# Performance work log

Hardware: AMD Instinct MI355X
Metric: run time of the kernel (lower is better)

Reference implementation:

```python
import jax, jax.numpy as jnp
import numpy as np
from jax import lax

T, B, D, H = 512, 64, 256, 512  # time, batch, input_dim, hidden_dim


def setup_inputs() -> dict:
    key = jax.random.key(0)
    ks = jax.random.split(key, 9)
    fan_in = D + H
    s = 1.0 / np.sqrt(fan_in)
    inputs = jax.random.normal(ks[0], (T, B, D), dtype=jnp.float32)
    # torch nn.Linear weight layout: [out_features, in_features]
    Wf = jax.random.uniform(ks[1], (H, fan_in), jnp.float32, -s, s)
    bf = jax.random.uniform(ks[2], (H,), jnp.float32, -s, s)
    Wi = jax.random.uniform(ks[3], (H, fan_in), jnp.float32, -s, s)
    bi = jax.random.uniform(ks[4], (H,), jnp.float32, -s, s)
    Wg = jax.random.uniform(ks[5], (H, fan_in), jnp.float32, -s, s)
    bg = jax.random.uniform(ks[6], (H,), jnp.float32, -s, s)
    Wo = jax.random.uniform(ks[7], (H, fan_in), jnp.float32, -s, s)
    bo = jax.random.uniform(ks[8], (H,), jnp.float32, -s, s)
    return {"inputs": inputs, "Wf": Wf, "bf": bf, "Wi": Wi, "bi": bi,
            "Wg": Wg, "bg": bg, "Wo": Wo, "bo": bo}


def reference(inputs, Wf, bf, Wi, bi, Wg, bg, Wo, bo):
    # LSTM-style gated recurrence, n_qubits=0 path (no depth loop, proj_back = Identity)
    batch = inputs.shape[1]
    hidden = bf.shape[0]
    h0 = jnp.zeros((batch, hidden), inputs.dtype)
    c0 = jnp.zeros((batch, hidden), inputs.dtype)

    def step(carry, x):
        hx, cx = carry
        comb = jnp.concatenate([x, hx], axis=1)  # [B, D+H]
        f = jax.nn.sigmoid(comb @ Wf.T + bf)
        i = jax.nn.sigmoid(comb @ Wi.T + bi)
        g = jnp.tanh(comb @ Wg.T + bg)
        o = jax.nn.sigmoid(comb @ Wo.T + bo)
        cx = f * cx + i * g
        hx = o * jnp.tanh(cx)
        return (hx, cx), hx

    (hx, cx), outputs = lax.scan(step, (h0, c0), inputs)
    return outputs, hx, cx
```

## Files before the change

### kernel.cpp

```cpp
#include <hip/hip_runtime.h>
#include <stdint.h>

#define T_STEPS 512
#define BATCH   64
#define DIN     256
#define HID     512
#define KTOT    768
#define NTEAMS  4
#define TB      16
#define KK_X    8
#define KK_H    16
#define KK_ALL  24

typedef __bf16 v8bf __attribute__((ext_vector_type(8)));
typedef float  v4f  __attribute__((ext_vector_type(4)));
typedef unsigned int v4u __attribute__((ext_vector_type(4)));

#define FLAGS_OFF 0
#define HBUF_OFF  8192
#define WPK_OFF   (HBUF_OFF + 131072)
#define XPK_OFF   (WPK_OFF + 3145728)

#define LOADH(d, a, IMM) \
  asm volatile("global_load_dwordx4 %0, %1, off offset:" IMM " sc0 sc1" \
               : "=v"(d) : "v"(a) : "memory")
#define STORE_SHORT_C(a, v) \
  asm volatile("global_store_short %0, %1, off sc0 sc1" :: "v"(a), "v"(v) : "memory")
#define STORE_DWORD_C(a, v) \
  asm volatile("global_store_dword %0, %1, off sc0 sc1" :: "v"(a), "v"(v) : "memory")
#define DRAIN_VM() asm volatile("s_waitcnt vmcnt(0)" ::: "memory")

static __device__ __forceinline__ unsigned short f2bf(float x) {
  union { float f; uint32_t u; } v; v.f = x;
  uint32_t r = (v.u + 0x7fffu + ((v.u >> 16) & 1u)) >> 16;
  return (unsigned short)r;
}

static __device__ __forceinline__ float sigm(float x) {
  float e = __builtin_amdgcn_exp2f(-1.44269504f * x);
  return __builtin_amdgcn_rcpf(1.0f + e);
}
static __device__ __forceinline__ float tanh_(float x) {
  float e = __builtin_amdgcn_exp2f(2.88539008f * x);
  return 1.0f - 2.0f * __builtin_amdgcn_rcpf(e + 1.0f);
}

__global__ void pack_w(const float* __restrict__ Wf, const float* __restrict__ Wi,
                       const float* __restrict__ Wg, const float* __restrict__ Wo,
                       unsigned short* __restrict__ wpk) {
  int n = blockIdx.x * 256 + threadIdx.x;
  int l  = n & 63;
  int kk = (n >> 6) % KK_ALL;
  int wv = (n >> 6) / KK_ALL;
  int row  = l & 15;
  int gate = row & 3;
  int unit = (wv >> 2) * 16 + (wv & 3) * 4 + (row >> 2);
  int col  = kk * 32 + (l >> 4) * 8;
  const float* W = (gate == 0) ? Wf : (gate == 1) ? Wi : (gate == 2) ? Wg : Wo;
  const float* src = W + (size_t)unit * KTOT + col;
  unsigned short* dst = wpk + (size_t)n * 8;
#pragma unroll
  for (int e = 0; e < 8; e++) dst[e] = f2bf(src[e]);
}

__global__ void pack_x(const float* __restrict__ X, unsigned short* __restrict__ xpk) {
  int n = blockIdx.x * 256 + threadIdx.x;
  int l    = n & 63;
  int kk   = (n >> 6) & 7;
  int team = (n >> 9) & 3;
  int t    = n >> 11;
  int b    = team * TB + (l & 15);
  int col  = kk * 32 + (l >> 4) * 8;
  const float* src = X + ((size_t)(t * BATCH + b)) * DIN + col;
  unsigned short* dst = xpk + (size_t)n * 8;
#pragma unroll
  for (int e = 0; e < 8; e++) dst[e] = f2bf(src[e]);
}

__global__ void __launch_bounds__(256, 1)
lstm_rec(const float* __restrict__ bf_, const float* __restrict__ bi_,
         const float* __restrict__ bg_, const float* __restrict__ bo_,
         const unsigned short* __restrict__ wpk, const unsigned short* __restrict__ xpk,
         float* __restrict__ out, unsigned int* flags, unsigned short* hbuf) {
  int blk  = blockIdx.x;
  int team = blk & 7;
  if (team >= NTEAMS) return;
  int cu  = blk >> 3;
  int tid = threadIdx.x;
  int w   = tid >> 6, l = tid & 63;
  int brow = l & 15;
  int ul   = l >> 4;
  int u    = cu * 16 + w * 4 + ul;
  int bglob = team * TB + brow;

  v4u wfu[KK_ALL];
  {
    const v4u* wp = (const v4u*)(wpk + ((size_t)(cu * 4 + w)) * (KK_ALL * 512) + l * 8);
#pragma unroll
    for (int kk = 0; kk < KK_ALL; kk++) wfu[kk] = wp[kk * 64];
#pragma unroll
    for (int kk = 0; kk < KK_ALL; kk++) asm volatile("" : "+v"(wfu[kk]));
  }
  float b0 = bf_[u], b1 = bi_[u], b2 = bg_[u], b3 = bo_[u];
  float c = 0.0f, hval = 0.0f;

  char* slab0 = (char*)(hbuf + (size_t)team * 2 * (TB * HID));
  char* slab1 = slab0 + TB * HID * 2;
  const char* cons0 = slab0 + brow * 1024 + ul * 16;
  const char* cons1 = slab1 + brow * 1024 + ul * 16;
  char* pub0 = slab0 + brow * 1024 + u * 2;
  char* pub1 = slab1 + brow * 1024 + u * 2;

  unsigned int* ftm = flags + (size_t)team * 32 * 16;
  unsigned int* myflag = ftm + (size_t)cu * 16;
  const unsigned int* pollp = ftm + (size_t)(l & 31) * 16;

  float* outb = out + (size_t)bglob * HID + u;

  for (int t = 0; t < T_STEPS; t++) {
    v8bf xf[KK_X];
    {
      const v8bf* xp = (const v8bf*)(xpk + ((size_t)(t * NTEAMS + team)) * (KK_X * 512) + l * 8);
#pragma unroll
      for (int kk = 0; kk < KK_X; kk++) xf[kk] = xp[kk * 64];
    }

    if (t > 0) {
      if (w == 0) {
        while (true) {
          unsigned int v = __hip_atomic_load(pollp, __ATOMIC_RELAXED, __HIP_MEMORY_SCOPE_AGENT);
          if (__all(v >= (unsigned)t)) break;
        }
      }
      __syncthreads();
    }

    const char* cb = (t & 1) ? cons1 : cons0;
    v4u hf[16];
    LOADH(hf[0],  cb, "0");   LOADH(hf[1],  cb, "64");
    LOADH(hf[2],  cb, "128"); LOADH(hf[3],  cb, "192");
    LOADH(hf[4],  cb, "256"); LOADH(hf[5],  cb, "320");
    LOADH(hf[6],  cb, "384"); LOADH(hf[7],  cb, "448");
    LOADH(hf[8],  cb, "512"); LOADH(hf[9],  cb, "576");
    LOADH(hf[10], cb, "640"); LOADH(hf[11], cb, "704");
    LOADH(hf[12], cb, "768"); LOADH(hf[13], cb, "832");
    LOADH(hf[14], cb, "896"); LOADH(hf[15], cb, "960");

    v4f acc[4];
    acc[0] = (v4f){b0, b1, b2, b3};
    acc[1] = (v4f){0.f, 0.f, 0.f, 0.f};
    acc[2] = (v4f){0.f, 0.f, 0.f, 0.f};
    acc[3] = (v4f){0.f, 0.f, 0.f, 0.f};
#pragma unroll
    for (int kk = 0; kk < KK_X; kk++)
      acc[kk & 3] = __builtin_amdgcn_mfma_f32_16x16x32_bf16(
          __builtin_bit_cast(v8bf, wfu[kk]), xf[kk], acc[kk & 3], 0, 0, 0);

    DRAIN_VM();
    __builtin_amdgcn_sched_barrier(0);

#pragma unroll
    for (int kk = 0; kk < KK_H; kk++)
      acc[kk & 3] = __builtin_amdgcn_mfma_f32_16x16x32_bf16(
          __builtin_bit_cast(v8bf, wfu[KK_X + kk]),
          __builtin_bit_cast(v8bf, hf[kk]), acc[kk & 3], 0, 0, 0);

    v4f g4 = (acc[0] + acc[1]) + (acc[2] + acc[3]);

    float fg = sigm(g4[0]);
    float ig = sigm(g4[1]);
    float gg = tanh_(g4[2]);
    float og = sigm(g4[3]);
    c    = fg * c + ig * gg;
    hval = og * tanh_(c);

    outb[(size_t)t * (BATCH * HID)] = hval;

    {
      char* pd = ((t + 1) & 1) ? pub1 : pub0;
      unsigned int hb = f2bf(hval);
      STORE_SHORT_C(pd, hb);
    }
    DRAIN_VM();
    __syncthreads();
    if (tid == 0) {
      unsigned int fv = (unsigned)(t + 1);
      STORE_DWORD_C(myflag, fv);
    }
  }

  float* hx = out + (size_t)T_STEPS * BATCH * HID;
  hx[(size_t)bglob * HID + u] = hval;
  float* cx = hx + BATCH * HID;
  cx[(size_t)bglob * HID + u] = c;
}

extern "C" void kernel_launch(void* const* d_in, const int* in_sizes, int n_in,
                              void* d_out, int out_size, void* d_ws, size_t ws_size,
                              hipStream_t stream) {
  const float* X  = (const float*)d_in[0];
  const float* Wf = (const float*)d_in[1];
  const float* bf = (const float*)d_in[2];
  const float* Wi = (const float*)d_in[3];
  const float* bi = (const float*)d_in[4];
  const float* Wg = (const float*)d_in[5];
  const float* bg = (const float*)d_in[6];
  const float* Wo = (const float*)d_in[7];
  const float* bo = (const float*)d_in[8];
  float* out = (float*)d_out;
  char* ws = (char*)d_ws;

  unsigned int*   flags = (unsigned int*)(ws + FLAGS_OFF);
  unsigned short* hbuf  = (unsigned short*)(ws + HBUF_OFF);
  unsigned short* wpk   = (unsigned short*)(ws + WPK_OFF);
  unsigned short* xpk   = (unsigned short*)(ws + XPK_OFF);

  hipMemsetAsync(ws, 0, WPK_OFF, stream);
  pack_w<<<768, 256, 0, stream>>>(Wf, Wi, Wg, Wo, wpk);
  pack_x<<<4096, 256, 0, stream>>>(X, xpk);
  lstm_rec<<<256, 256, 0, stream>>>(bf, bi, bg, bo, wpk, xpk, out, flags, hbuf);
}
```

Baseline: 1.652 ms.

## Stage recurrent h through LDS with coalesced loads and packed publishes

Each wave now loads one quarter of the team's h slab with four coalesced device-scope loads and writes it into swizzled shared memory. All waves then read their MFMA B fragments from LDS, so each wave no longer issues sixteen scattered global loads. On the publish side, values are gathered with shuffles so 16 lanes each write one packed 8-byte store instead of every lane storing a short. Cache-scope bits drop from sc0 sc1 to sc1, the publish and flag write are skipped on the last step, and a bounded poll loop is added; the extra __syncthreads and the weaker coherence scope are the main risks.

```diff
diff --git a/kernel.cpp b/kernel.cpp
--- a/kernel.cpp
+++ b/kernel.cpp
@@ -12,23 +12,35 @@
 #define KK_H    16
 #define KK_ALL  24
 
+#define POLL_BOUND (1 << 18)
+
 typedef __bf16 v8bf __attribute__((ext_vector_type(8)));
 typedef float  v4f  __attribute__((ext_vector_type(4)));
 typedef unsigned int v4u __attribute__((ext_vector_type(4)));
+typedef unsigned int v2u __attribute__((ext_vector_type(2)));
 
 #define FLAGS_OFF 0
 #define HBUF_OFF  8192
 #define WPK_OFF   (HBUF_OFF + 131072)
 #define XPK_OFF   (WPK_OFF + 3145728)
 
-#define LOADH(d, a, IMM) \
-  asm volatile("global_load_dwordx4 %0, %1, off offset:" IMM " sc0 sc1" \
+#define LOADX4_DEV(d, a, IMM) \
+  asm volatile("global_load_dwordx4 %0, %1, off offset:" IMM " sc1" \
                : "=v"(d) : "v"(a) : "memory")
-#define STORE_SHORT_C(a, v) \
-  asm volatile("global_store_short %0, %1, off sc0 sc1" :: "v"(a), "v"(v) : "memory")
-#define STORE_DWORD_C(a, v) \
-  asm volatile("global_store_dword %0, %1, off sc0 sc1" :: "v"(a), "v"(v) : "memory")
+#define ST2_DEV(a, v) \
+  asm volatile("global_store_dwordx2 %0, %1, off sc1" :: "v"(a), "v"(v) : "memory")
+#define ST_DW_DEV(a, v) \
+  asm volatile("global_store_dword %0, %1, off sc1" :: "v"(a), "v"(v) : "memory")
+#define LOADX4(d, a) \
+  asm volatile("global_load_dwordx4 %0, %1, off" : "=v"(d) : "v"(a) : "memory")
 #define DRAIN_VM() asm volatile("s_waitcnt vmcnt(0)" ::: "memory")
+
+static __device__ __forceinline__ unsigned int ld_flag_dev(const unsigned int* p) {
+  unsigned int v;
+  asm volatile("global_load_dword %0, %1, off sc1\n\ts_waitcnt vmcnt(0)"
+               : "=v"(v) : "v"(p) : "memory");
+  return v;
+}
 
 static __device__ __forceinline__ unsigned short f2bf(float x) {
   union { float f; uint32_t u; } v; v.f = x;
@@ -93,27 +105,24 @@
   int u    = cu * 16 + w * 4 + ul;
   int bglob = team * TB + brow;
 
+  __shared__ v4u hls[1024];
+  char* hl = (char*)hls;
+
   v4u wfu[KK_ALL];
   {
-    const v4u* wp = (const v4u*)(wpk + ((size_t)(cu * 4 + w)) * (KK_ALL * 512) + l * 8);
-#pragma unroll
-    for (int kk = 0; kk < KK_ALL; kk++) wfu[kk] = wp[kk * 64];
-#pragma unroll
-    for (int kk = 0; kk < KK_ALL; kk++) asm volatile("" : "+v"(wfu[kk]));
+    const char* wp = (const char*)(wpk + ((size_t)(cu * 4 + w)) * (KK_ALL * 512) + l * 8);
+#pragma unroll
+    for (int kk = 0; kk < KK_ALL; kk++) LOADX4(wfu[kk], wp + (size_t)kk * 1024);
+    DRAIN_VM();
   }
   float b0 = bf_[u], b1 = bi_[u], b2 = bg_[u], b3 = bo_[u];
   float c = 0.0f, hval = 0.0f;
 
   char* slab0 = (char*)(hbuf + (size_t)team * 2 * (TB * HID));
   char* slab1 = slab0 + TB * HID * 2;
-  const char* cons0 = slab0 + brow * 1024 + ul * 16;
-  const char* cons1 = slab1 + brow * 1024 + ul * 16;
-  char* pub0 = slab0 + brow * 1024 + u * 2;
-  char* pub1 = slab1 + brow * 1024 + u * 2;
 
   unsigned int* ftm = flags + (size_t)team * 32 * 16;
   unsigned int* myflag = ftm + (size_t)cu * 16;
-  const unsigned int* pollp = ftm + (size_t)(l & 31) * 16;
 
   float* outb = out + (size_t)bglob * HID + u;
 
@@ -127,24 +136,25 @@
 
     if (t > 0) {
       if (w == 0) {
+        const unsigned int* pp = ftm + (size_t)(l & 31) * 16;
+        int guard = 0;
         while (true) {
-          unsigned int v = __hip_atomic_load(pollp, __ATOMIC_RELAXED, __HIP_MEMORY_SCOPE_AGENT);
+          unsigned int v = ld_flag_dev(pp);
           if (__all(v >= (unsigned)t)) break;
+          if (++guard > POLL_BOUND) break;
         }
       }
       __syncthreads();
     }
 
-    const char* cb = (t & 1) ? cons1 : cons0;
-    v4u hf[16];
-    LOADH(hf[0],  cb, "0");   LOADH(hf[1],  cb, "64");
-    LOADH(hf[2],  cb, "128"); LOADH(hf[3],  cb, "192");
-    LOADH(hf[4],  cb, "256"); LOADH(hf[5],  cb, "320");
-    LOADH(hf[6],  cb, "384"); LOADH(hf[7],  cb, "448");
-    LOADH(hf[8],  cb, "512"); LOADH(hf[9],  cb, "576");
-    LOADH(hf[10], cb, "640"); LOADH(hf[11], cb, "704");
-    LOADH(hf[12], cb, "768"); LOADH(hf[13], cb, "832");
-    LOADH(hf[14], cb, "896"); LOADH(hf[15], cb, "960");
+    v4u s0, s1, s2, s3;
+    {
+      const char* sb = ((t & 1) ? slab1 : slab0) + w * 4096 + l * 16;
+      LOADX4_DEV(s0, sb, "0");
+      LOADX4_DEV(s1, sb, "1024");
+      LOADX4_DEV(s2, sb, "2048");
+      LOADX4_DEV(s3, sb, "3072");
+    }
 
     v4f acc[4];
     acc[0] = (v4f){b0, b1, b2, b3};
@@ -159,12 +169,22 @@
     DRAIN_VM();
     __builtin_amdgcn_sched_barrier(0);
 
-#pragma unroll
-    for (int kk = 0; kk < KK_H; kk++)
+    {
+      int r = w * 4;
+      *(v4u*)(hl + (((r + 0) * 1024 + l * 16) ^ (((r + 0) & 7) << 4))) = s0;
+      *(v4u*)(hl + (((r + 1) * 1024 + l * 16) ^ (((r + 1) & 7) << 4))) = s1;
+      *(v4u*)(hl + (((r + 2) * 1024 + l * 16) ^ (((r + 2) & 7) << 4))) = s2;
+      *(v4u*)(hl + (((r + 3) * 1024 + l * 16) ^ (((r + 3) & 7) << 4))) = s3;
+    }
+    __syncthreads();
+
+#pragma unroll
+    for (int kk = 0; kk < KK_H; kk++) {
+      int off = (brow * 1024 + kk * 64 + ul * 16) ^ ((brow & 7) << 4);
+      v8bf hf = *(const v8bf*)(hl + off);
       acc[kk & 3] = __builtin_amdgcn_mfma_f32_16x16x32_bf16(
-          __builtin_bit_cast(v8bf, wfu[KK_X + kk]),
-          __builtin_bit_cast(v8bf, hf[kk]), acc[kk & 3], 0, 0, 0);
-
+          __builtin_bit_cast(v8bf, wfu[KK_X + kk]), hf, acc[kk & 3], 0, 0, 0);
+    }
     v4f g4 = (acc[0] + acc[1]) + (acc[2] + acc[3]);
 
     float fg = sigm(g4[0]);
@@ -174,19 +194,24 @@
     c    = fg * c + ig * gg;
     hval = og * tanh_(c);
 
+    if (t < T_STEPS - 1) {
+      float h0 = __shfl(hval, brow);
+      float h1 = __shfl(hval, brow + 16);
+      float h2 = __shfl(hval, brow + 32);
+      float h3 = __shfl(hval, brow + 48);
+      if (l < 16) {
+        v2u pk;
+        pk.x = (unsigned)f2bf(h0) | ((unsigned)f2bf(h1) << 16);
+        pk.y = (unsigned)f2bf(h2) | ((unsigned)f2bf(h3) << 16);
+        char* pd = (((t + 1) & 1) ? slab1 : slab0) + brow * 1024 + cu * 32 + w * 8;
+        ST2_DEV(pd, pk);
+      }
+      DRAIN_VM();
+      __syncthreads();
+      if (tid == 0) ST_DW_DEV(myflag, (unsigned)(t + 1));
+    }
+
     outb[(size_t)t * (BATCH * HID)] = hval;
-
-    {
-      char* pd = ((t + 1) & 1) ? pub1 : pub0;
-      unsigned int hb = f2bf(hval);
-      STORE_SHORT_C(pd, hb);
-    }
-    DRAIN_VM();
-    __syncthreads();
-    if (tid == 0) {
-      unsigned int fv = (unsigned)(t + 1);
-      STORE_DWORD_C(myflag, fv);
-    }
   }
 
   float* hx = out + (size_t)T_STEPS * BATCH * HID;
```

Measured after the change: 1.348 ms. 18.4% less time.
